# Kernel optimization log

Hardware: AMD Instinct MI355X
Metric: run time of the kernel (lower is better)

Reference implementation:

```python
import jax, jax.numpy as jnp
import numpy as np

EMB = 384
RANK = 8


def feature2token(f):
    # [B,C,H,W] -> [B,HW,C]
    B, C, H, W = f.shape
    return f.reshape(B, C, H * W).transpose(0, 2, 1)


def token2feature(t, H, W):
    # [B,N,C] -> [B,C,H,W]
    B, N, C = t.shape
    return t.transpose(0, 2, 1).reshape(B, C, H, W)


def linear(t, w, b):
    # torch Linear: y = t @ w.T + b ; w: [out,in]
    return jnp.einsum('bnc,oc->bno', t, w) + b


def hard_mask(y_soft, k):
    # straight-through one-hot mask of the top-k entries of y_soft, per row
    B, N = y_soft.shape
    idx = jax.lax.top_k(y_soft, k)[1]                      # [B,k]
    y_hard = jnp.zeros_like(y_soft).at[jnp.arange(B)[:, None], idx].set(1.0)
    return y_hard - jax.lax.stop_gradient(y_soft) + y_soft


def gumbel_masks(scores, k):
    # scores: [B,N] raw logits; module applies log_softmax then softmax
    y_soft = jax.nn.softmax(jax.nn.log_softmax(scores, axis=-1), axis=-1)
    token_mask = hard_mask(y_soft, k)        # top-k
    rej_mask = hard_mask(-y_soft, k) + 2.0 * jax.lax.stop_gradient(y_soft) - 2.0 * y_soft
    # note: rej uses topk of (-y_soft) for indices but straight-through around +y_soft,
    # so compute it directly for clarity:
    B, N = y_soft.shape
    idx_bot = jax.lax.top_k(-y_soft, k)[1]
    y_hard_bot = jnp.zeros_like(y_soft).at[jnp.arange(B)[:, None], idx_bot].set(1.0)
    rej_mask = y_hard_bot - jax.lax.stop_gradient(y_soft) + y_soft
    return token_mask, rej_mask


def setup_inputs() -> dict:
    key = jax.random.key(0)
    ks = jax.random.split(key, 20)
    B, C, H, W = 32, EMB, 32, 32
    s_emb = 1.0 / np.sqrt(EMB)
    s_2r = 1.0 / np.sqrt(2 * RANK)
    s_r = 1.0 / np.sqrt(RANK)
    inp = {
        'x': jax.random.normal(ks[0], (B, 2 * C, H, W), jnp.float32),
        'gx_w': jax.random.uniform(ks[1], (1, EMB), jnp.float32, -s_emb, s_emb),
        'gx_b': jax.random.uniform(ks[2], (1,), jnp.float32, -s_emb, s_emb),
        'gm_w': jax.random.uniform(ks[3], (1, EMB), jnp.float32, -s_emb, s_emb),
        'gm_b': jax.random.uniform(ks[4], (1,), jnp.float32, -s_emb, s_emb),
        'px_w': jax.random.uniform(ks[5], (RANK, EMB), jnp.float32, -s_emb, s_emb),
        'px_b': jax.random.uniform(ks[6], (RANK,), jnp.float32, -s_emb, s_emb),
        'pm_w': jax.random.uniform(ks[7], (RANK, EMB), jnp.float32, -s_emb, s_emb),
        'pm_b': jax.random.uniform(ks[8], (RANK,), jnp.float32, -s_emb, s_emb),
        'prx_w': jax.random.uniform(ks[9], (RANK, EMB), jnp.float32, -s_emb, s_emb),
        'prx_b': jax.random.uniform(ks[10], (RANK,), jnp.float32, -s_emb, s_emb),
        'prm_w': jax.random.uniform(ks[11], (RANK, EMB), jnp.float32, -s_emb, s_emb),
        'prm_b': jax.random.uniform(ks[12], (RANK,), jnp.float32, -s_emb, s_emb),
        'pfx_w': jax.random.uniform(ks[13], (RANK, 2 * RANK), jnp.float32, -s_2r, s_2r),
        'pfx_b': jax.random.uniform(ks[14], (RANK,), jnp.float32, -s_2r, s_2r),
        'pfm_w': jax.random.uniform(ks[15], (RANK, 2 * RANK), jnp.float32, -s_2r, s_2r),
        'pfm_b': jax.random.uniform(ks[16], (RANK,), jnp.float32, -s_2r, s_2r),
        'pb_w': jax.random.uniform(ks[17], (EMB, RANK), jnp.float32, -s_r, s_r),
        'pb_b': jax.random.uniform(ks[18], (EMB,), jnp.float32, -s_r, s_r),
    }
    return inp


def reference(x, gx_w, gx_b, gm_w, gm_b, px_w, px_b, pm_w, pm_b,
              prx_w, prx_b, prm_w, prm_b, pfx_w, pfx_b, pfm_w, pfm_b,
              pb_w, pb_b):
    xh, modh = jnp.split(x, 2, axis=1)           # each [B,C,H,W]
    H, W = xh.shape[2], xh.shape[3]
    xt = feature2token(xh)                        # [B,N,C]
    mt = feature2token(modh)
    B, N, _ = xt.shape
    k = N // 4

    # x-branch
    scores_x = linear(xt, gx_w, gx_b).reshape(B, N)
    tm_x, rm_x = gumbel_masks(scores_x, k)
    tm_x, rm_x = tm_x[..., None], rm_x[..., None]             # [B,N,1] broadcast over emb
    low_x = linear(xt * tm_x + mt * rm_x, px_w, px_b)
    low_res_x = linear((xt + mt) * (1.0 - rm_x - tm_x), prx_w, prx_b)
    fuse_x = linear(jnp.concatenate([low_x, low_res_x], axis=2), pfx_w, pfx_b)

    # mod-branch
    scores_m = linear(mt, gm_w, gm_b).reshape(B, N)
    tm_m, rm_m = gumbel_masks(scores_m, k)
    tm_m, rm_m = tm_m[..., None], rm_m[..., None]
    low_m = linear(mt * tm_m + xt * rm_m, pm_w, pm_b)
    low_res_m = linear((xt + mt) * (1.0 - rm_m - tm_m), prm_w, prm_b)
    fuse_m = linear(jnp.concatenate([low_m, low_res_m], axis=2), pfm_w, pfm_b)

    fuse = linear(fuse_x + fuse_m, pb_w, pb_b)   # [B,N,EMB]
    return token2feature(fuse, H, W)
```

## Files before the change

### kernel.cpp

```cpp
#include <hip/hip_runtime.h>

#define NTOK 1024
#define KSEL 256


template <int NS>
__global__ __launch_bounds__(128) void k1_proj(
    const float* __restrict__ x,
    const float* __restrict__ gx_w, const float* __restrict__ gm_w,
    const float* __restrict__ px_w, const float* __restrict__ pm_w,
    const float* __restrict__ prx_w, const float* __restrict__ prm_w,
    float* __restrict__ Pp)
{
  constexpr int CS = 384 / NS;
  constexpr int SB = (NS == 8) ? 3 : (NS == 4) ? 2 : 0;
  int blk = blockIdx.x;
  int part = blk & 1;
  int ntile = (blk >> 1) & 3;
  int s = (blk >> 3) & (NS - 1);
  int b = blk >> (3 + SB);
  int n0 = ntile * 256 + threadIdx.x * 2;
  const float* gw = part ? gm_w : gx_w;
  int cw0 = s * CS;

  float2 acc[33];
  #pragma unroll
  for (int j = 0; j < 33; ++j) { acc[j].x = 0.f; acc[j].y = 0.f; }

  const float* xp = x + ((size_t)b * 768 + part * 384 + cw0) * NTOK + n0;
  #pragma unroll 8
  for (int c = 0; c < CS; ++c) {
    float2 v = *reinterpret_cast<const float2*>(xp + (size_t)c * NTOK);
    int cw = cw0 + c;
    float w0 = gw[cw];
    acc[0].x = fmaf(w0, v.x, acc[0].x);
    acc[0].y = fmaf(w0, v.y, acc[0].y);
    #pragma unroll
    for (int r = 0; r < 8; ++r) {
      float wa = px_w[r * 384 + cw];
      float wb = pm_w[r * 384 + cw];
      float wc = prx_w[r * 384 + cw];
      float wd = prm_w[r * 384 + cw];
      acc[1 + r].x  = fmaf(wa, v.x, acc[1 + r].x);
      acc[1 + r].y  = fmaf(wa, v.y, acc[1 + r].y);
      acc[9 + r].x  = fmaf(wb, v.x, acc[9 + r].x);
      acc[9 + r].y  = fmaf(wb, v.y, acc[9 + r].y);
      acc[17 + r].x = fmaf(wc, v.x, acc[17 + r].x);
      acc[17 + r].y = fmaf(wc, v.y, acc[17 + r].y);
      acc[25 + r].x = fmaf(wd, v.x, acc[25 + r].x);
      acc[25 + r].y = fmaf(wd, v.y, acc[25 + r].y);
    }
  }
  float* op = Pp + ((((size_t)s * 32 + b) * 2 + part) * 33) * NTOK + n0;
  #pragma unroll
  for (int j = 0; j < 33; ++j)
    *reinterpret_cast<float2*>(op + (size_t)j * NTOK) = acc[j];
}

__global__ __launch_bounds__(64) void k2_masks(
    const float* __restrict__ Ppart, float* __restrict__ masks, int nsplit)
{
  int b = blockIdx.x >> 1;
  int branch = blockIdx.x & 1;
  int lane = threadIdx.x;
  unsigned long long lmask = (1ull << lane) - 1ull;

  float v[16];
  #pragma unroll
  for (int i = 0; i < 16; ++i) v[i] = 0.f;
  for (int s = 0; s < nsplit; ++s) {
    const float* sp = Ppart + (((size_t)s * 32 + b) * 2 + branch) * 33 * NTOK;
    #pragma unroll
    for (int i = 0; i < 16; ++i) v[i] += sp[i * 64 + lane];
  }
  unsigned key[16];
  #pragma unroll
  for (int i = 0; i < 16; ++i) {
    float f = v[i] + 0.0f;
    unsigned bits = __float_as_uint(f);
    key[i] = (bits & 0x80000000u) ? ~bits : (bits | 0x80000000u);
  }

  for (int which = 0; which < 2; ++which) {
    unsigned prefix = 0u;
    for (int bit = 31; bit >= 0; --bit) {
      unsigned cand = prefix | (1u << bit);
      int cnt = 0;
      #pragma unroll
      for (int i = 0; i < 16; ++i) {
        unsigned kk = which ? ~key[i] : key[i];
        cnt += __popcll(__ballot(kk >= cand));
      }
      if (cnt >= KSEL) prefix = cand;
    }
    int cgt = 0;
    #pragma unroll
    for (int i = 0; i < 16; ++i) {
      unsigned kk = which ? ~key[i] : key[i];
      cgt += __popcll(__ballot(kk > prefix));
    }
    int quota = KSEL - cgt;
    float* mp = masks + ((size_t)b * 4 + branch * 2 + which) * NTOK;
    int run = 0;
    #pragma unroll
    for (int i = 0; i < 16; ++i) {
      unsigned kk = which ? ~key[i] : key[i];
      bool eq = (kk == prefix);
      unsigned long long bal = __ballot(eq);
      int rank = run + __popcll(bal & lmask);
      bool sel = (kk > prefix) || (eq && rank < quota);
      mp[i * 64 + lane] = sel ? 1.0f : 0.0f;
      run += __popcll(bal);
    }
  }
}

template <int NS>
__global__ __launch_bounds__(256) void k3f(
    const float* __restrict__ Ppart, const float* __restrict__ masks,
    const float* __restrict__ px_b, const float* __restrict__ pm_b,
    const float* __restrict__ prx_b, const float* __restrict__ prm_b,
    const float* __restrict__ pfx_w, const float* __restrict__ pfx_b,
    const float* __restrict__ pfm_w, const float* __restrict__ pfm_b,
    const float* __restrict__ pb_w, const float* __restrict__ pb_b,
    float* __restrict__ out)
{
  __shared__ float lows[32][64];
  __shared__ float gl[8][64];
  int tile = blockIdx.x & 15;
  int b = blockIdx.x >> 4;
  int t = threadIdx.x;
  int tok = t & 63;
  int kind = t >> 6;
  int n = tile * 64 + tok;

  int branch = kind >> 1;
  const float* mk = masks + ((size_t)b * 4 + branch * 2) * NTOK + n;
  float tm = mk[0];
  float rm = mk[NTOK];
  int rowbase = (kind == 0) ? 1 : (kind == 1) ? 17 : (kind == 2) ? 9 : 25;

  #pragma unroll
  for (int r = 0; r < 8; ++r) {
    float s0 = 0.f, s1 = 0.f;
    #pragma unroll
    for (int sp = 0; sp < NS; ++sp) {
      const float* P0 = Ppart + (((size_t)sp * 32 + b) * 2 + 0) * 33 * NTOK + n;
      const float* P1 = Ppart + (((size_t)sp * 32 + b) * 2 + 1) * 33 * NTOK + n;
      s0 += P0[(size_t)(rowbase + r) * NTOK];
      s1 += P1[(size_t)(rowbase + r) * NTOK];
    }
    float val;
    if (kind == 0)      val = fmaf(tm, s0, fmaf(rm, s1, px_b[r]));
    else if (kind == 2) val = fmaf(tm, s1, fmaf(rm, s0, pm_b[r]));
    else {
      float w = 1.0f - tm - rm;
      val = fmaf(w, s0 + s1, (kind == 1) ? prx_b[r] : prm_b[r]);
    }
    lows[kind * 8 + r][tok] = val;
  }
  __syncthreads();

  if (t < 64) {
    float L[32];
    #pragma unroll
    for (int i = 0; i < 32; ++i) L[i] = lows[i][tok];
    #pragma unroll
    for (int r = 0; r < 8; ++r) {
      float acc = pfx_b[r] + pfm_b[r];
      #pragma unroll
      for (int s2 = 0; s2 < 8; ++s2) {
        acc = fmaf(pfx_w[r * 16 + s2],     L[s2],      acc);
        acc = fmaf(pfx_w[r * 16 + 8 + s2], L[8 + s2],  acc);
        acc = fmaf(pfm_w[r * 16 + s2],     L[16 + s2], acc);
        acc = fmaf(pfm_w[r * 16 + 8 + s2], L[24 + s2], acc);
      }
      gl[r][tok] = acc;
    }
  }
  __syncthreads();

  float g[8];
  #pragma unroll
  for (int r = 0; r < 8; ++r) g[r] = gl[r][tok];

  float* op = out + ((size_t)b * 384 + (size_t)kind * 96) * NTOK + n;
  const float* wp = pb_w + (size_t)kind * 96 * 8;
  const float* bp = pb_b + (size_t)kind * 96;
  #pragma unroll 4
  for (int c = 0; c < 96; ++c) {
    const float* w = wp + c * 8;
    float acc = bp[c];
    acc = fmaf(w[0], g[0], acc);
    acc = fmaf(w[1], g[1], acc);
    acc = fmaf(w[2], g[2], acc);
    acc = fmaf(w[3], g[3], acc);
    acc = fmaf(w[4], g[4], acc);
    acc = fmaf(w[5], g[5], acc);
    acc = fmaf(w[6], g[6], acc);
    acc = fmaf(w[7], g[7], acc);
    op[(size_t)c * NTOK] = acc;
  }
}

extern "C" void kernel_launch(void* const* d_in, const int* in_sizes, int n_in,
                              void* d_out, int out_size, void* d_ws, size_t ws_size,
                              hipStream_t stream) {
  const float* x     = (const float*)d_in[0];
  const float* gx_w  = (const float*)d_in[1];
  const float* gm_w  = (const float*)d_in[3];
  const float* px_w  = (const float*)d_in[5];
  const float* px_b  = (const float*)d_in[6];
  const float* pm_w  = (const float*)d_in[7];
  const float* pm_b  = (const float*)d_in[8];
  const float* prx_w = (const float*)d_in[9];
  const float* prx_b = (const float*)d_in[10];
  const float* prm_w = (const float*)d_in[11];
  const float* prm_b = (const float*)d_in[12];
  const float* pfx_w = (const float*)d_in[13];
  const float* pfx_b = (const float*)d_in[14];
  const float* pfm_w = (const float*)d_in[15];
  const float* pfm_b = (const float*)d_in[16];
  const float* pb_w  = (const float*)d_in[17];
  const float* pb_b  = (const float*)d_in[18];
  float* out = (float*)d_out;

  const size_t P1_F   = 32ull * 2 * 33 * NTOK;
  const size_t MASK_F = 32ull * 4 * NTOK;
  const size_t need4  = (4 * P1_F + MASK_F) * 4;

  float* ws = (float*)d_ws;
  if (ws_size >= need4) {
    float* Ppart = ws;
    float* masks = ws + 4 * P1_F;
    k1_proj<4><<<1024, 128, 0, stream>>>(x, gx_w, gm_w, px_w, pm_w, prx_w, prm_w, Ppart);
    k2_masks<<<64, 64, 0, stream>>>(Ppart, masks, 4);
    k3f<4><<<512, 256, 0, stream>>>(Ppart, masks, px_b, pm_b, prx_b, prm_b,
                                    pfx_w, pfx_b, pfm_w, pfm_b, pb_w, pb_b, out);
  } else {
    float* Ppart = ws;
    float* masks = ws + P1_F;
    k1_proj<1><<<256, 128, 0, stream>>>(x, gx_w, gm_w, px_w, pm_w, prx_w, prm_w, Ppart);
    k2_masks<<<64, 64, 0, stream>>>(Ppart, masks, 1);
    k3f<1><<<512, 256, 0, stream>>>(Ppart, masks, px_b, pm_b, prx_b, prm_b,
                                    pfx_w, pfx_b, pfm_w, pfm_b, pb_w, pb_b, out);
  }
}
```

Baseline: 274.8 us.

## Stage projection weights in LDS, widen token tiles, split output projection kernel

The projection kernel now loads its 33 weight rows into shared memory and processes four tokens per thread with float4 loads, four channels per step. This replaces repeated scalar global weight reads with LDS reads and raises arithmetic per load. The channel split goes from 4 to 8 when workspace allows. The final 8->384 projection moves into its own kernel, so the whole output write is spread over more blocks, at the cost of an extra launch and a round trip of the intermediate through global memory. The 33 float4 accumulators greatly increase register pressure.

```diff
diff --git a/kernel.cpp b/kernel.cpp
--- a/kernel.cpp
+++ b/kernel.cpp
@@ -5,7 +5,7 @@
 
 
 template <int NS>
-__global__ __launch_bounds__(128) void k1_proj(
+__global__ __launch_bounds__(128, 2) void k1_proj(
     const float* __restrict__ x,
     const float* __restrict__ gx_w, const float* __restrict__ gm_w,
     const float* __restrict__ px_w, const float* __restrict__ pm_w,
@@ -13,48 +13,55 @@
     float* __restrict__ Pp)
 {
   constexpr int CS = 384 / NS;
-  constexpr int SB = (NS == 8) ? 3 : (NS == 4) ? 2 : 0;
+  constexpr int L2NS = (NS == 8) ? 3 : 2;
+  __shared__ float wlds[33 * CS];
+
   int blk = blockIdx.x;
   int part = blk & 1;
-  int ntile = (blk >> 1) & 3;
-  int s = (blk >> 3) & (NS - 1);
-  int b = blk >> (3 + SB);
-  int n0 = ntile * 256 + threadIdx.x * 2;
+  int ntile = (blk >> 1) & 1;
+  int s = (blk >> 2) & (NS - 1);
+  int b = blk >> (2 + L2NS);
+  int n0 = ntile * 512 + threadIdx.x * 4;
   const float* gw = part ? gm_w : gx_w;
   int cw0 = s * CS;
 
-  float2 acc[33];
-  #pragma unroll
-  for (int j = 0; j < 33; ++j) { acc[j].x = 0.f; acc[j].y = 0.f; }
+  for (int idx = threadIdx.x; idx < 33 * CS; idx += 128) {
+    int j = idx / CS;
+    int c = idx - j * CS;
+    const float* src;
+    if (j == 0)       src = gw + cw0;
+    else if (j < 9)   src = px_w  + (j - 1)  * 384 + cw0;
+    else if (j < 17)  src = pm_w  + (j - 9)  * 384 + cw0;
+    else if (j < 25)  src = prx_w + (j - 17) * 384 + cw0;
+    else              src = prm_w + (j - 25) * 384 + cw0;
+    wlds[idx] = src[c];
+  }
+  __syncthreads();
+
+  float4 acc[33];
+  #pragma unroll
+  for (int j = 0; j < 33; ++j) acc[j] = make_float4(0.f, 0.f, 0.f, 0.f);
 
   const float* xp = x + ((size_t)b * 768 + part * 384 + cw0) * NTOK + n0;
-  #pragma unroll 8
-  for (int c = 0; c < CS; ++c) {
-    float2 v = *reinterpret_cast<const float2*>(xp + (size_t)c * NTOK);
-    int cw = cw0 + c;
-    float w0 = gw[cw];
-    acc[0].x = fmaf(w0, v.x, acc[0].x);
-    acc[0].y = fmaf(w0, v.y, acc[0].y);
-    #pragma unroll
-    for (int r = 0; r < 8; ++r) {
-      float wa = px_w[r * 384 + cw];
-      float wb = pm_w[r * 384 + cw];
-      float wc = prx_w[r * 384 + cw];
-      float wd = prm_w[r * 384 + cw];
-      acc[1 + r].x  = fmaf(wa, v.x, acc[1 + r].x);
-      acc[1 + r].y  = fmaf(wa, v.y, acc[1 + r].y);
-      acc[9 + r].x  = fmaf(wb, v.x, acc[9 + r].x);
-      acc[9 + r].y  = fmaf(wb, v.y, acc[9 + r].y);
-      acc[17 + r].x = fmaf(wc, v.x, acc[17 + r].x);
-      acc[17 + r].y = fmaf(wc, v.y, acc[17 + r].y);
-      acc[25 + r].x = fmaf(wd, v.x, acc[25 + r].x);
-      acc[25 + r].y = fmaf(wd, v.y, acc[25 + r].y);
+  #pragma unroll 2
+  for (int c4 = 0; c4 < CS / 4; ++c4) {
+    float4 v0 = *reinterpret_cast<const float4*>(xp + (size_t)(c4 * 4 + 0) * NTOK);
+    float4 v1 = *reinterpret_cast<const float4*>(xp + (size_t)(c4 * 4 + 1) * NTOK);
+    float4 v2 = *reinterpret_cast<const float4*>(xp + (size_t)(c4 * 4 + 2) * NTOK);
+    float4 v3 = *reinterpret_cast<const float4*>(xp + (size_t)(c4 * 4 + 3) * NTOK);
+    #pragma unroll
+    for (int j = 0; j < 33; ++j) {
+      float4 w = *reinterpret_cast<const float4*>(&wlds[j * CS + c4 * 4]);
+      acc[j].x = fmaf(w.x, v0.x, fmaf(w.y, v1.x, fmaf(w.z, v2.x, fmaf(w.w, v3.x, acc[j].x))));
+      acc[j].y = fmaf(w.x, v0.y, fmaf(w.y, v1.y, fmaf(w.z, v2.y, fmaf(w.w, v3.y, acc[j].y))));
+      acc[j].z = fmaf(w.x, v0.z, fmaf(w.y, v1.z, fmaf(w.z, v2.z, fmaf(w.w, v3.z, acc[j].z))));
+      acc[j].w = fmaf(w.x, v0.w, fmaf(w.y, v1.w, fmaf(w.z, v2.w, fmaf(w.w, v3.w, acc[j].w))));
     }
   }
   float* op = Pp + ((((size_t)s * 32 + b) * 2 + part) * 33) * NTOK + n0;
   #pragma unroll
   for (int j = 0; j < 33; ++j)
-    *reinterpret_cast<float2*>(op + (size_t)j * NTOK) = acc[j];
+    *reinterpret_cast<float4*>(op + (size_t)j * NTOK) = acc[j];
 }
 
 __global__ __launch_bounds__(64) void k2_masks(
@@ -116,17 +123,15 @@
 }
 
 template <int NS>
-__global__ __launch_bounds__(256) void k3f(
+__global__ __launch_bounds__(256) void k3g(
     const float* __restrict__ Ppart, const float* __restrict__ masks,
     const float* __restrict__ px_b, const float* __restrict__ pm_b,
     const float* __restrict__ prx_b, const float* __restrict__ prm_b,
     const float* __restrict__ pfx_w, const float* __restrict__ pfx_b,
     const float* __restrict__ pfm_w, const float* __restrict__ pfm_b,
-    const float* __restrict__ pb_w, const float* __restrict__ pb_b,
-    float* __restrict__ out)
+    float* __restrict__ G)
 {
   __shared__ float lows[32][64];
-  __shared__ float gl[8][64];
   int tile = blockIdx.x & 15;
   int b = blockIdx.x >> 4;
   int t = threadIdx.x;
@@ -175,30 +180,45 @@
         acc = fmaf(pfm_w[r * 16 + s2],     L[16 + s2], acc);
         acc = fmaf(pfm_w[r * 16 + 8 + s2], L[24 + s2], acc);
       }
-      gl[r][tok] = acc;
-    }
-  }
+      G[((size_t)b * 8 + r) * NTOK + n] = acc;
+    }
+  }
+}
+
+__global__ __launch_bounds__(256) void k4_out(
+    const float* __restrict__ G, const float* __restrict__ pb_w,
+    const float* __restrict__ pb_b, float* __restrict__ out)
+{
+  __shared__ float wl[48 * 8 + 48];
+  int blk = blockIdx.x;
+  int ttile = blk & 3;
+  int cpart = (blk >> 2) & 7;
+  int b = blk >> 5;
+  int c0 = cpart * 48;
+
+  for (int idx = threadIdx.x; idx < 48 * 8 + 48; idx += 256)
+    wl[idx] = (idx < 384) ? pb_w[(size_t)c0 * 8 + idx] : pb_b[c0 + idx - 384];
   __syncthreads();
 
+  int n = ttile * 256 + threadIdx.x;
   float g[8];
   #pragma unroll
-  for (int r = 0; r < 8; ++r) g[r] = gl[r][tok];
-
-  float* op = out + ((size_t)b * 384 + (size_t)kind * 96) * NTOK + n;
-  const float* wp = pb_w + (size_t)kind * 96 * 8;
-  const float* bp = pb_b + (size_t)kind * 96;
+  for (int r = 0; r < 8; ++r) g[r] = G[((size_t)b * 8 + r) * NTOK + n];
+
+  float* op = out + ((size_t)b * 384 + c0) * NTOK + n;
   #pragma unroll 4
-  for (int c = 0; c < 96; ++c) {
-    const float* w = wp + c * 8;
-    float acc = bp[c];
-    acc = fmaf(w[0], g[0], acc);
-    acc = fmaf(w[1], g[1], acc);
-    acc = fmaf(w[2], g[2], acc);
-    acc = fmaf(w[3], g[3], acc);
-    acc = fmaf(w[4], g[4], acc);
-    acc = fmaf(w[5], g[5], acc);
-    acc = fmaf(w[6], g[6], acc);
-    acc = fmaf(w[7], g[7], acc);
+  for (int c = 0; c < 48; ++c) {
+    float4 w0 = *reinterpret_cast<const float4*>(&wl[c * 8]);
+    float4 w1 = *reinterpret_cast<const float4*>(&wl[c * 8 + 4]);
+    float acc = wl[384 + c];
+    acc = fmaf(w0.x, g[0], acc);
+    acc = fmaf(w0.y, g[1], acc);
+    acc = fmaf(w0.z, g[2], acc);
+    acc = fmaf(w0.w, g[3], acc);
+    acc = fmaf(w1.x, g[4], acc);
+    acc = fmaf(w1.y, g[5], acc);
+    acc = fmaf(w1.z, g[6], acc);
+    acc = fmaf(w1.w, g[7], acc);
     op[(size_t)c * NTOK] = acc;
   }
 }
@@ -227,22 +247,28 @@
 
   const size_t P1_F   = 32ull * 2 * 33 * NTOK;
   const size_t MASK_F = 32ull * 4 * NTOK;
-  const size_t need4  = (4 * P1_F + MASK_F) * 4;
+  const size_t G_F    = 32ull * 8 * NTOK;
+  const size_t need8  = (8 * P1_F + MASK_F + G_F) * 4;
+  const size_t need4  = (4 * P1_F + MASK_F + G_F) * 4;
 
   float* ws = (float*)d_ws;
-  if (ws_size >= need4) {
+  if (ws_size >= need8) {
+    float* Ppart = ws;
+    float* masks = ws + 8 * P1_F;
+    float* G     = masks + MASK_F;
+    k1_proj<8><<<1024, 128, 0, stream>>>(x, gx_w, gm_w, px_w, pm_w, prx_w, prm_w, Ppart);
+    k2_masks<<<64, 64, 0, stream>>>(Ppart, masks, 8);
+    k3g<8><<<512, 256, 0, stream>>>(Ppart, masks, px_b, pm_b, prx_b, prm_b,
+                                    pfx_w, pfx_b, pfm_w, pfm_b, G);
+    k4_out<<<1024, 256, 0, stream>>>(G, pb_w, pb_b, out);
+  } else {
     float* Ppart = ws;
     float* masks = ws + 4 * P1_F;
-    k1_proj<4><<<1024, 128, 0, stream>>>(x, gx_w, gm_w, px_w, pm_w, prx_w, prm_w, Ppart);
+    float* G     = masks + MASK_F;
+    k1_proj<4><<<512, 128, 0, stream>>>(x, gx_w, gm_w, px_w, pm_w, prx_w, prm_w, Ppart);
     k2_masks<<<64, 64, 0, stream>>>(Ppart, masks, 4);
-    k3f<4><<<512, 256, 0, stream>>>(Ppart, masks, px_b, pm_b, prx_b, prm_b,
-                                    pfx_w, pfx_b, pfm_w, pfm_b, pb_w, pb_b, out);
-  } else {
-    float* Ppart = ws;
-    float* masks = ws + P1_F;
-    k1_proj<1><<<256, 128, 0, stream>>>(x, gx_w, gm_w, px_w, pm_w, prx_w, prm_w, Ppart);
-    k2_masks<<<64, 64, 0, stream>>>(Ppart, masks, 1);
-    k3f<1><<<512, 256, 0, stream>>>(Ppart, masks, px_b, pm_b, prx_b, prm_b,
-                                    pfx_w, pfx_b, pfm_w, pfm_b, pb_w, pb_b, out);
-  }
-}
+    k3g<4><<<512, 256, 0, stream>>>(Ppart, masks, px_b, pm_b, prx_b, prm_b,
+                                    pfx_w, pfx_b, pfm_w, pfm_b, G);
+    k4_out<<<1024, 256, 0, stream>>>(G, pb_w, pb_b, out);
+  }
+}
```

Result: faster. 250.3 us (-8.9%).
